# Kernel tuning notes

Hardware: AMD Instinct MI355X
Metric: run time of the kernel (lower is better)

Reference implementation:

```python
import jax, jax.numpy as jnp
import numpy as np

N_C = 64
D = 128

def setup_inputs() -> dict:
    key = jax.random.key(0)
    embeddings = jax.random.normal(key, (1024, N_C * D), dtype=jnp.float32)
    return {"embeddings": embeddings}

def reference(embeddings) -> jnp.ndarray:
    two_b, _ = embeddings.shape
    B = two_b // 2
    # (2, B, n_c, d), softmax over last dim
    q = jax.nn.softmax(embeddings.reshape(2, B, N_C, D), axis=-1)
    q_a, q_b = q[0], q[1]  # (B, n_c, d)

    self_sim_loss = -(q_a * q_b).sum() / (B * N_C)

    q_a2 = q_a * q_a
    q_b2 = q_b * q_b
    # Faithful to the repeat/repeat_interleave + bmm: block (i, j) of the
    # (n_c^2, d, d) product equals q2[:, j].T @ q2[:, i]  -> einsum over batch.
    prod_a = jnp.einsum('bjc,bid->ijcd', q_a2, q_a2)  # (n_c, n_c, d, d)
    prod_b = jnp.einsum('bjc,bid->ijcd', q_b2, q_b2)

    # mask out diagonal cluster pairs i == j (done before sqrt in original;
    # entries are strictly positive so masking after sqrt is identical)
    offdiag = (~jnp.eye(N_C, dtype=bool))[:, :, None, None]  # (n_c, n_c, 1, 1)

    raw_a = jnp.where(offdiag, jnp.sqrt(prod_a), 0.0).sum()
    raw_b = jnp.where(offdiag, jnp.sqrt(prod_b), 0.0).sum()

    scale = (N_C * N_C - N_C) * (B ** 0.5)
    cluster_loss = -(raw_a / scale + raw_b / scale) / 2
    return self_sim_loss + cluster_loss
```

## Files before the change

kernel.cpp:

```cpp
#include <hip/hip_runtime.h>
#include <cstdint>
#include <cstddef>

#define NCLUS 64
#define DIM   128
#define BATCH 512
#define QCOLS 8192
#define NPAIR 2016
#define TSTRB (QCOLS * BATCH)
#define FP8SCALE 256.0f

typedef float f32x16 __attribute__((ext_vector_type(16)));
typedef int   i32x4  __attribute__((ext_vector_type(4)));
typedef int   i32x8  __attribute__((ext_vector_type(8)));


__device__ __forceinline__ void ld_lds16(const void* g, void* l) {
  __builtin_amdgcn_global_load_lds(
      (__attribute__((address_space(1))) void*)g,
      (__attribute__((address_space(3))) void*)l, 16, 0, 0);
}

#define SYNC_VM4()  asm volatile("s_waitcnt vmcnt(4)\n\ts_barrier" ::: "memory")
#define SYNC_VM0()  asm volatile("s_waitcnt vmcnt(0)\n\ts_barrier" ::: "memory")
#define SYNC_LGKM() asm volatile("s_waitcnt lgkmcnt(0)\n\ts_barrier" ::: "memory")

__global__ __launch_bounds__(256) void softmax_q2_kernel(
    const float* __restrict__ emb, uint8_t* __restrict__ q2t,
    float* __restrict__ dotPart) {
  __shared__ uint32_t T32[2 * 64 * 33];
  __shared__ float red[4];
  const int c  = blockIdx.y;
  const int bq = blockIdx.x;
  const int tid = threadIdx.x;
  const int w = tid >> 6, lane = tid & 63;
  const int sub = lane >> 5;
  const int col = lane & 31;

  float4 qa = {0.f, 0.f, 0.f, 0.f};
  float dot = 0.f;

#pragma unroll
  for (int k = 0; k < 16; ++k) {
    const int t  = k & 1;
    const int bl = w * 16 + (k >> 1) * 2 + sub;
    const int b  = bq * 64 + bl;
    const float4 v = *(const float4*)(emb +
        ((size_t)(t * BATCH + b) * QCOLS + (size_t)c * DIM + col * 4));

    float mx = fmaxf(fmaxf(v.x, v.y), fmaxf(v.z, v.w));
#pragma unroll
    for (int off = 1; off < 32; off <<= 1) mx = fmaxf(mx, __shfl_xor(mx, off));
    float e0 = __expf(v.x - mx), e1 = __expf(v.y - mx);
    float e2 = __expf(v.z - mx), e3 = __expf(v.w - mx);
    float s = (e0 + e1) + (e2 + e3);
#pragma unroll
    for (int off = 1; off < 32; off <<= 1) s += __shfl_xor(s, off);
    const float inv = 1.0f / s;
    const float q0 = e0 * inv, q1 = e1 * inv, q2 = e2 * inv, q3 = e3 * inv;

    if (t == 0) { qa.x = q0; qa.y = q1; qa.z = q2; qa.w = q3; }
    else        { dot += qa.x * q0 + qa.y * q1 + qa.z * q2 + qa.w * q3; }

    int pk = __builtin_amdgcn_cvt_pk_fp8_f32(q0 * q0 * FP8SCALE,
                                             q1 * q1 * FP8SCALE, 0, false);
    pk = __builtin_amdgcn_cvt_pk_fp8_f32(q2 * q2 * FP8SCALE,
                                         q3 * q3 * FP8SCALE, pk, true);
    T32[(t * 64 + bl) * 33 + col] = (uint32_t)pk;
  }
  __syncthreads();

#pragma unroll
  for (int it = 0; it < 4; ++it) {
    int ch = it * 256 + tid;
    int t = ch >> 9, d = (ch >> 2) & 127, b16 = ch & 3;
    const int dq = d >> 2, sh = (d & 3) * 8;
    uint32_t w0 = 0, w1 = 0, w2 = 0, w3 = 0;
#pragma unroll
    for (int r = 0; r < 4; ++r) {
      w0 |= ((T32[(t * 64 + b16 * 16 +  0 + r) * 33 + dq] >> sh) & 0xFFu) << (8 * r);
      w1 |= ((T32[(t * 64 + b16 * 16 +  4 + r) * 33 + dq] >> sh) & 0xFFu) << (8 * r);
      w2 |= ((T32[(t * 64 + b16 * 16 +  8 + r) * 33 + dq] >> sh) & 0xFFu) << (8 * r);
      w3 |= ((T32[(t * 64 + b16 * 16 + 12 + r) * 33 + dq] >> sh) & 0xFFu) << (8 * r);
    }
    size_t off = (size_t)t * TSTRB + (size_t)(c * DIM + d) * BATCH +
                 (size_t)bq * 64 + b16 * 16;
    uint4 o; o.x = w0; o.y = w1; o.z = w2; o.w = w3;
    *(uint4*)(q2t + off) = o;
  }

#pragma unroll
  for (int off = 1; off < 64; off <<= 1) dot += __shfl_xor(dot, off);
  if (lane == 0) red[w] = dot;
  __syncthreads();
  if (tid == 0) dotPart[blockIdx.y * 8 + blockIdx.x] = red[0] + red[1] + red[2] + red[3];
}

__global__ __launch_bounds__(256, 4) void gram_sqrt_kernel(
    const uint8_t* __restrict__ q2t, float* __restrict__ Spart) {
  __shared__ uint8_t L[32768 + 16];

  int sidx = ((int)blockIdx.x & 7) * 252 + ((int)blockIdx.x >> 3);
  int q = sidx, gi = 0;
  while (q >= 64 * gi + 28) { q -= 64 * gi + 28; ++gi; }
  int I, J;
  if (q < 64 * gi) {
    int gj = q >> 6, r = q & 63;
    I = gi * 8 + (r >> 3);
    J = gj * 8 + (r & 7);
  } else {
    int dq = q - 64 * gi;
    int il = 1;
    while (il * (il + 1) / 2 <= dq) ++il;
    I = gi * 8 + il;
    J = gi * 8 + (dq - il * (il - 1) / 2);
  }

  const uint8_t* baseA = q2t + (size_t)J * (DIM * BATCH);
  const uint8_t* baseB = q2t + (size_t)I * (DIM * BATCH);

  const int tid  = threadIdx.x;
  const int lane = tid & 63, w = tid >> 6;
  const int wm = w & 1, wn = w >> 1;

  const int t0 = tid, t1 = 256 + tid;
  const int r0s = t0 >> 2, r1s = t1 >> 2;
  const int rot0 = (r0s + (r0s >> 2)) & 3;
  const int rot1 = (r1s + (r1s >> 2)) & 3;
  const int c0s = ((t0 & 3) - rot0) & 3;
  const int c1s = ((t1 & 3) - rot1) & 3;
  const size_t g0 = (size_t)r0s * BATCH + c0s * 16;
  const size_t g1 = (size_t)r1s * BATCH + c1s * 16;
  uint8_t* Lb = L;
  const int ldsw = w * 1024;

  const int h = lane >> 5, r31 = lane & 31;
  const int rot = (r31 + (r31 >> 2)) & 3;
  const int ro1 = ((2 * h + rot) & 3) * 16;
  const int ro2 = ((2 * h + 1 + rot) & 3) * 16;
  const int ArowO = (wm * 64 + r31) * 64;
  const int BrowO = 8192 + (wn * 64 + r31) * 64;

  f32x16 acc[2][2];
#pragma unroll
  for (int i = 0; i < 2; ++i)
#pragma unroll
    for (int j = 0; j < 2; ++j) acc[i][j] = (f32x16)(0.f);

  float S0 = 0.f, S1 = 0.f;

  ld_lds16(baseA + g0, Lb + ldsw);
  ld_lds16(baseA + g1, Lb + 4096 + ldsw);
  ld_lds16(baseB + g0, Lb + 8192 + ldsw);
  ld_lds16(baseB + g1, Lb + 12288 + ldsw);

  for (int m = 0; m < 16; ++m) {
    if (m < 15) {
      const int mi = m + 1;
      const int bb = (mi & 1) << 14;
      const size_t ck = (size_t)(mi >> 3) * TSTRB + (size_t)(mi & 7) * 64;
      ld_lds16(baseA + ck + g0, Lb + bb + ldsw);
      ld_lds16(baseA + ck + g1, Lb + bb + 4096 + ldsw);
      ld_lds16(baseB + ck + g0, Lb + bb + 8192 + ldsw);
      ld_lds16(baseB + ck + g1, Lb + bb + 12288 + ldsw);
      SYNC_VM4();
    } else {
      SYNC_VM0();
    }

    const int be = (m & 1) << 14;
    i32x4 alo[2], ahi[2], blo[2], bhi[2];
#pragma unroll
    for (int g = 0; g < 2; ++g) {
      alo[g] = *(const i32x4*)(Lb + be + ArowO + g * 2048 + ro1);
      ahi[g] = *(const i32x4*)(Lb + be + ArowO + g * 2048 + ro2);
      blo[g] = *(const i32x4*)(Lb + be + BrowO + g * 2048 + ro1);
      bhi[g] = *(const i32x4*)(Lb + be + BrowO + g * 2048 + ro2);
    }
    i32x8 af[2], bf[2];
#pragma unroll
    for (int g = 0; g < 2; ++g) {
      af[g] = (i32x8){alo[g].x, alo[g].y, alo[g].z, alo[g].w,
                      ahi[g].x, ahi[g].y, ahi[g].z, ahi[g].w};
      bf[g] = (i32x8){blo[g].x, blo[g].y, blo[g].z, blo[g].w,
                      bhi[g].x, bhi[g].y, bhi[g].z, bhi[g].w};
    }
#pragma unroll
    for (int i = 0; i < 2; ++i)
#pragma unroll
      for (int j = 0; j < 2; ++j)
        acc[i][j] = __builtin_amdgcn_mfma_scale_f32_32x32x64_f8f6f4(
            af[i], bf[j], acc[i][j], 0, 0, 0, 0x7F7F7F7F, 0, 0x7F7F7F7F);

    if (m == 7) {
#pragma unroll
      for (int i = 0; i < 2; ++i)
#pragma unroll
        for (int j = 0; j < 2; ++j) {
#pragma unroll
          for (int e = 0; e < 16; ++e) S0 += sqrtf(acc[i][j][e]);
          acc[i][j] = (f32x16)(0.f);
        }
    }

    SYNC_LGKM();
  }

#pragma unroll
  for (int i = 0; i < 2; ++i)
#pragma unroll
    for (int j = 0; j < 2; ++j)
#pragma unroll
      for (int e = 0; e < 16; ++e) S1 += sqrtf(acc[i][j][e]);

  float local = (S0 + S1) * (1.0f / 256.0f);
#pragma unroll
  for (int off = 1; off < 64; off <<= 1) local += __shfl_xor(local, off);
  float* fred = (float*)(L + 32768);
  if (lane == 0) fred[w] = local;
  __syncthreads();
  if (tid == 0) Spart[blockIdx.x] = fred[0] + fred[1] + fred[2] + fred[3];
}

__global__ __launch_bounds__(256) void finalize_kernel(
    const float* __restrict__ P, float* __restrict__ out) {
  __shared__ float rd[8];
  const int tid = threadIdx.x;
  float d = 0.f, s = 0.f;
  for (int i = tid; i < 512; i += 256) d += P[i];
  for (int i = tid; i < NPAIR; i += 256) s += P[512 + i];
#pragma unroll
  for (int off = 1; off < 64; off <<= 1) { d += __shfl_xor(d, off); s += __shfl_xor(s, off); }
  const int w = tid >> 6;
  if ((tid & 63) == 0) { rd[w] = d; rd[4 + w] = s; }
  __syncthreads();
  if (tid == 0) {
    float dt = rd[0] + rd[1] + rd[2] + rd[3];
    float st = rd[4] + rd[5] + rd[6] + rd[7];
    out[0] = -dt / 32768.0f - st / (4032.0f * 22.62741699796952f);
  }
}

extern "C" void kernel_launch(void* const* d_in, const int* in_sizes, int n_in,
                              void* d_out, int out_size, void* d_ws, size_t ws_size,
                              hipStream_t stream) {
  const float* emb = (const float*)d_in[0];
  float* out = (float*)d_out;
  float* P = (float*)d_ws;
  uint8_t* q2t = (uint8_t*)d_ws + 16384;

  softmax_q2_kernel<<<dim3(8, 64), 256, 0, stream>>>(emb, q2t, P);
  gram_sqrt_kernel<<<dim3(NPAIR), 256, 0, stream>>>(q2t, P + 512);
  finalize_kernel<<<1, 256, 0, stream>>>(P, out);
}
```

Before: 127.5 us.

## Load gram MFMA operands directly from global into registers, shrink softmax blocks

The gram kernel no longer stages fp8 tiles through LDS with async global-to-LDS loads and barriers. Each wave now loads its MFMA fragments straight from global memory into registers, double-buffered across 8 K-chunks of 128 bytes, which removes the LDS round trip and per-iteration barriers. The softmax kernel is split into 4x more blocks, each handling 16 batch rows, to raise parallelism, and the finalize offsets are adjusted to match. The costs are more register pressure from the 32 i32x4 fragment registers, less coalesced global reads, and loss of cross-wave operand sharing, so A and B tiles are fetched redundantly per wave.

```diff
diff --git a/kernel.cpp b/kernel.cpp
--- a/kernel.cpp
+++ b/kernel.cpp
@@ -15,20 +15,10 @@
 typedef int   i32x8  __attribute__((ext_vector_type(8)));
 
 
-__device__ __forceinline__ void ld_lds16(const void* g, void* l) {
-  __builtin_amdgcn_global_load_lds(
-      (__attribute__((address_space(1))) void*)g,
-      (__attribute__((address_space(3))) void*)l, 16, 0, 0);
-}
-
-#define SYNC_VM4()  asm volatile("s_waitcnt vmcnt(4)\n\ts_barrier" ::: "memory")
-#define SYNC_VM0()  asm volatile("s_waitcnt vmcnt(0)\n\ts_barrier" ::: "memory")
-#define SYNC_LGKM() asm volatile("s_waitcnt lgkmcnt(0)\n\ts_barrier" ::: "memory")
-
 __global__ __launch_bounds__(256) void softmax_q2_kernel(
     const float* __restrict__ emb, uint8_t* __restrict__ q2t,
     float* __restrict__ dotPart) {
-  __shared__ uint32_t T32[2 * 64 * 33];
+  __shared__ uint32_t T32[2 * 16 * 33];
   __shared__ float red[4];
   const int c  = blockIdx.y;
   const int bq = blockIdx.x;
@@ -41,10 +31,10 @@
   float dot = 0.f;
 
 #pragma unroll
-  for (int k = 0; k < 16; ++k) {
+  for (int k = 0; k < 4; ++k) {
     const int t  = k & 1;
-    const int bl = w * 16 + (k >> 1) * 2 + sub;
-    const int b  = bq * 64 + bl;
+    const int bl = w * 4 + (k >> 1) * 2 + sub;
+    const int b  = bq * 16 + bl;
     const float4 v = *(const float4*)(emb +
         ((size_t)(t * BATCH + b) * QCOLS + (size_t)c * DIM + col * 4));
 
@@ -66,25 +56,23 @@
                                              q1 * q1 * FP8SCALE, 0, false);
     pk = __builtin_amdgcn_cvt_pk_fp8_f32(q2 * q2 * FP8SCALE,
                                          q3 * q3 * FP8SCALE, pk, true);
-    T32[(t * 64 + bl) * 33 + col] = (uint32_t)pk;
-  }
-  __syncthreads();
-
-#pragma unroll
-  for (int it = 0; it < 4; ++it) {
-    int ch = it * 256 + tid;
-    int t = ch >> 9, d = (ch >> 2) & 127, b16 = ch & 3;
+    T32[(t * 16 + bl) * 33 + col] = (uint32_t)pk;
+  }
+  __syncthreads();
+
+  {
+    const int t = tid >> 7, d = tid & 127;
     const int dq = d >> 2, sh = (d & 3) * 8;
     uint32_t w0 = 0, w1 = 0, w2 = 0, w3 = 0;
 #pragma unroll
     for (int r = 0; r < 4; ++r) {
-      w0 |= ((T32[(t * 64 + b16 * 16 +  0 + r) * 33 + dq] >> sh) & 0xFFu) << (8 * r);
-      w1 |= ((T32[(t * 64 + b16 * 16 +  4 + r) * 33 + dq] >> sh) & 0xFFu) << (8 * r);
-      w2 |= ((T32[(t * 64 + b16 * 16 +  8 + r) * 33 + dq] >> sh) & 0xFFu) << (8 * r);
-      w3 |= ((T32[(t * 64 + b16 * 16 + 12 + r) * 33 + dq] >> sh) & 0xFFu) << (8 * r);
+      w0 |= ((T32[(t * 16 +  0 + r) * 33 + dq] >> sh) & 0xFFu) << (8 * r);
+      w1 |= ((T32[(t * 16 +  4 + r) * 33 + dq] >> sh) & 0xFFu) << (8 * r);
+      w2 |= ((T32[(t * 16 +  8 + r) * 33 + dq] >> sh) & 0xFFu) << (8 * r);
+      w3 |= ((T32[(t * 16 + 12 + r) * 33 + dq] >> sh) & 0xFFu) << (8 * r);
     }
     size_t off = (size_t)t * TSTRB + (size_t)(c * DIM + d) * BATCH +
-                 (size_t)bq * 64 + b16 * 16;
+                 (size_t)bq * 16;
     uint4 o; o.x = w0; o.y = w1; o.z = w2; o.w = w3;
     *(uint4*)(q2t + off) = o;
   }
@@ -93,12 +81,12 @@
   for (int off = 1; off < 64; off <<= 1) dot += __shfl_xor(dot, off);
   if (lane == 0) red[w] = dot;
   __syncthreads();
-  if (tid == 0) dotPart[blockIdx.y * 8 + blockIdx.x] = red[0] + red[1] + red[2] + red[3];
-}
-
-__global__ __launch_bounds__(256, 4) void gram_sqrt_kernel(
+  if (tid == 0) dotPart[c * 32 + bq] = red[0] + red[1] + red[2] + red[3];
+}
+
+__global__ __launch_bounds__(256) void gram_sqrt_kernel(
     const uint8_t* __restrict__ q2t, float* __restrict__ Spart) {
-  __shared__ uint8_t L[32768 + 16];
+  __shared__ float red[4];
 
   int sidx = ((int)blockIdx.x & 7) * 252 + ((int)blockIdx.x >> 3);
   int q = sidx, gi = 0;
@@ -116,30 +104,19 @@
     J = gi * 8 + (dq - il * (il - 1) / 2);
   }
 
-  const uint8_t* baseA = q2t + (size_t)J * (DIM * BATCH);
-  const uint8_t* baseB = q2t + (size_t)I * (DIM * BATCH);
+  const uint8_t* __restrict__ pA = q2t + (size_t)J * (DIM * BATCH);
+  const uint8_t* __restrict__ pB = q2t + (size_t)I * (DIM * BATCH);
 
   const int tid  = threadIdx.x;
   const int lane = tid & 63, w = tid >> 6;
   const int wm = w & 1, wn = w >> 1;
-
-  const int t0 = tid, t1 = 256 + tid;
-  const int r0s = t0 >> 2, r1s = t1 >> 2;
-  const int rot0 = (r0s + (r0s >> 2)) & 3;
-  const int rot1 = (r1s + (r1s >> 2)) & 3;
-  const int c0s = ((t0 & 3) - rot0) & 3;
-  const int c1s = ((t1 & 3) - rot1) & 3;
-  const size_t g0 = (size_t)r0s * BATCH + c0s * 16;
-  const size_t g1 = (size_t)r1s * BATCH + c1s * 16;
-  uint8_t* Lb = L;
-  const int ldsw = w * 1024;
-
   const int h = lane >> 5, r31 = lane & 31;
-  const int rot = (r31 + (r31 >> 2)) & 3;
-  const int ro1 = ((2 * h + rot) & 3) * 16;
-  const int ro2 = ((2 * h + 1 + rot) & 3) * 16;
-  const int ArowO = (wm * 64 + r31) * 64;
-  const int BrowO = 8192 + (wn * 64 + r31) * 64;
+  const uint32_t kb = (uint32_t)h * 32u;
+
+  const uint32_t oA0 = (uint32_t)(wm * 64 +  0 + r31) * BATCH + kb;
+  const uint32_t oA1 = (uint32_t)(wm * 64 + 32 + r31) * BATCH + kb;
+  const uint32_t oB0 = (uint32_t)(wn * 64 +  0 + r31) * BATCH + kb;
+  const uint32_t oB1 = (uint32_t)(wn * 64 + 32 + r31) * BATCH + kb;
 
   f32x16 acc[2][2];
 #pragma unroll
@@ -147,52 +124,57 @@
 #pragma unroll
     for (int j = 0; j < 2; ++j) acc[i][j] = (f32x16)(0.f);
 
+  i32x4 fr[2][16];
+
+#define CHOFF(p) ((size_t)((p) >> 2) * TSTRB + (size_t)((p) & 3) * 128)
+#define LD16(ptr) (*(const i32x4*)(ptr))
+#define ISSUE(sl, p) do {                                                   \
+    const uint8_t* ap = pA + CHOFF(p);                                      \
+    const uint8_t* bp = pB + CHOFF(p);                                      \
+    fr[sl][ 0] = LD16(ap + oA0);      fr[sl][ 1] = LD16(ap + oA0 + 16);     \
+    fr[sl][ 2] = LD16(ap + oA0 + 64); fr[sl][ 3] = LD16(ap + oA0 + 80);     \
+    fr[sl][ 4] = LD16(ap + oA1);      fr[sl][ 5] = LD16(ap + oA1 + 16);     \
+    fr[sl][ 6] = LD16(ap + oA1 + 64); fr[sl][ 7] = LD16(ap + oA1 + 80);     \
+    fr[sl][ 8] = LD16(bp + oB0);      fr[sl][ 9] = LD16(bp + oB0 + 16);     \
+    fr[sl][10] = LD16(bp + oB0 + 64); fr[sl][11] = LD16(bp + oB0 + 80);     \
+    fr[sl][12] = LD16(bp + oB1);      fr[sl][13] = LD16(bp + oB1 + 16);     \
+    fr[sl][14] = LD16(bp + oB1 + 64); fr[sl][15] = LD16(bp + oB1 + 80);     \
+  } while (0)
+
+#define MFMA(a, b, c) __builtin_amdgcn_mfma_scale_f32_32x32x64_f8f6f4(        \
+    (a), (b), (c), 0, 0, 0, 0x7F7F7F7F, 0, 0x7F7F7F7F)
+#define CAT8(lo, hi) __builtin_shufflevector((lo), (hi), 0, 1, 2, 3, 4, 5, 6, 7)
+
   float S0 = 0.f, S1 = 0.f;
 
-  ld_lds16(baseA + g0, Lb + ldsw);
-  ld_lds16(baseA + g1, Lb + 4096 + ldsw);
-  ld_lds16(baseB + g0, Lb + 8192 + ldsw);
-  ld_lds16(baseB + g1, Lb + 12288 + ldsw);
-
-  for (int m = 0; m < 16; ++m) {
-    if (m < 15) {
-      const int mi = m + 1;
-      const int bb = (mi & 1) << 14;
-      const size_t ck = (size_t)(mi >> 3) * TSTRB + (size_t)(mi & 7) * 64;
-      ld_lds16(baseA + ck + g0, Lb + bb + ldsw);
-      ld_lds16(baseA + ck + g1, Lb + bb + 4096 + ldsw);
-      ld_lds16(baseB + ck + g0, Lb + bb + 8192 + ldsw);
-      ld_lds16(baseB + ck + g1, Lb + bb + 12288 + ldsw);
-      SYNC_VM4();
-    } else {
-      SYNC_VM0();
-    }
-
-    const int be = (m & 1) << 14;
-    i32x4 alo[2], ahi[2], blo[2], bhi[2];
-#pragma unroll
-    for (int g = 0; g < 2; ++g) {
-      alo[g] = *(const i32x4*)(Lb + be + ArowO + g * 2048 + ro1);
-      ahi[g] = *(const i32x4*)(Lb + be + ArowO + g * 2048 + ro2);
-      blo[g] = *(const i32x4*)(Lb + be + BrowO + g * 2048 + ro1);
-      bhi[g] = *(const i32x4*)(Lb + be + BrowO + g * 2048 + ro2);
-    }
-    i32x8 af[2], bf[2];
-#pragma unroll
-    for (int g = 0; g < 2; ++g) {
-      af[g] = (i32x8){alo[g].x, alo[g].y, alo[g].z, alo[g].w,
-                      ahi[g].x, ahi[g].y, ahi[g].z, ahi[g].w};
-      bf[g] = (i32x8){blo[g].x, blo[g].y, blo[g].z, blo[g].w,
-                      bhi[g].x, bhi[g].y, bhi[g].z, bhi[g].w};
-    }
-#pragma unroll
-    for (int i = 0; i < 2; ++i)
-#pragma unroll
-      for (int j = 0; j < 2; ++j)
-        acc[i][j] = __builtin_amdgcn_mfma_scale_f32_32x32x64_f8f6f4(
-            af[i], bf[j], acc[i][j], 0, 0, 0, 0x7F7F7F7F, 0, 0x7F7F7F7F);
-
-    if (m == 7) {
+  ISSUE(0, 0);
+#pragma unroll
+  for (int p = 0; p < 8; ++p) {
+    if (p < 7) ISSUE((p + 1) & 1, p + 1);
+    const int sl = p & 1;
+
+    {
+      i32x8 a0 = CAT8(fr[sl][0],  fr[sl][1]);
+      i32x8 a1 = CAT8(fr[sl][4],  fr[sl][5]);
+      i32x8 b0 = CAT8(fr[sl][8],  fr[sl][9]);
+      i32x8 b1 = CAT8(fr[sl][12], fr[sl][13]);
+      acc[0][0] = MFMA(a0, b0, acc[0][0]);
+      acc[0][1] = MFMA(a0, b1, acc[0][1]);
+      acc[1][0] = MFMA(a1, b0, acc[1][0]);
+      acc[1][1] = MFMA(a1, b1, acc[1][1]);
+    }
+    {
+      i32x8 a0 = CAT8(fr[sl][2],  fr[sl][3]);
+      i32x8 a1 = CAT8(fr[sl][6],  fr[sl][7]);
+      i32x8 b0 = CAT8(fr[sl][10], fr[sl][11]);
+      i32x8 b1 = CAT8(fr[sl][14], fr[sl][15]);
+      acc[0][0] = MFMA(a0, b0, acc[0][0]);
+      acc[0][1] = MFMA(a0, b1, acc[0][1]);
+      acc[1][0] = MFMA(a1, b0, acc[1][0]);
+      acc[1][1] = MFMA(a1, b1, acc[1][1]);
+    }
+
+    if (p == 3) {
 #pragma unroll
       for (int i = 0; i < 2; ++i)
 #pragma unroll
@@ -202,8 +184,6 @@
           acc[i][j] = (f32x16)(0.f);
         }
     }
-
-    SYNC_LGKM();
   }
 
 #pragma unroll
@@ -216,10 +196,9 @@
   float local = (S0 + S1) * (1.0f / 256.0f);
 #pragma unroll
   for (int off = 1; off < 64; off <<= 1) local += __shfl_xor(local, off);
-  float* fred = (float*)(L + 32768);
-  if (lane == 0) fred[w] = local;
-  __syncthreads();
-  if (tid == 0) Spart[blockIdx.x] = fred[0] + fred[1] + fred[2] + fred[3];
+  if (lane == 0) red[w] = local;
+  __syncthreads();
+  if (tid == 0) Spart[blockIdx.x] = red[0] + red[1] + red[2] + red[3];
 }
 
 __global__ __launch_bounds__(256) void finalize_kernel(
@@ -227,8 +206,8 @@
   __shared__ float rd[8];
   const int tid = threadIdx.x;
   float d = 0.f, s = 0.f;
-  for (int i = tid; i < 512; i += 256) d += P[i];
-  for (int i = tid; i < NPAIR; i += 256) s += P[512 + i];
+  for (int i = tid; i < 2048; i += 256) d += P[i];
+  for (int i = tid; i < NPAIR; i += 256) s += P[2048 + i];
 #pragma unroll
   for (int off = 1; off < 64; off <<= 1) { d += __shfl_xor(d, off); s += __shfl_xor(s, off); }
   const int w = tid >> 6;
@@ -249,7 +228,7 @@
   float* P = (float*)d_ws;
   uint8_t* q2t = (uint8_t*)d_ws + 16384;
 
-  softmax_q2_kernel<<<dim3(8, 64), 256, 0, stream>>>(emb, q2t, P);
-  gram_sqrt_kernel<<<dim3(NPAIR), 256, 0, stream>>>(q2t, P + 512);
+  softmax_q2_kernel<<<dim3(32, 64), 256, 0, stream>>>(emb, q2t, P);
+  gram_sqrt_kernel<<<dim3(NPAIR), 256, 0, stream>>>(q2t, P + 2048);
   finalize_kernel<<<1, 256, 0, stream>>>(P, out);
 }
```

Result: slower. 202.6 us (+58.9%).

## Triple-buffer gram LDS pipeline, drop trailing barrier, widen softmax blocks

Applied to the files above, without the earlier changes.

The gram kernel moves from a double-buffered to a triple-buffered LDS pipeline with prefetch distance two. Each iteration now needs only one vmcnt wait plus barrier, because the end-of-iteration lgkmcnt barrier is gone, and the MFMA block runs at raised wave priority. The cost is 48KB of LDS per block and the loss of the 4-blocks-per-CU launch bound, which may lower occupancy. The softmax kernel also switches to 512-thread blocks, each doing half as many rows per thread.

```diff
diff --git a/kernel.cpp b/kernel.cpp
--- a/kernel.cpp
+++ b/kernel.cpp
@@ -21,15 +21,14 @@
       (__attribute__((address_space(3))) void*)l, 16, 0, 0);
 }
 
-#define SYNC_VM4()  asm volatile("s_waitcnt vmcnt(4)\n\ts_barrier" ::: "memory")
-#define SYNC_VM0()  asm volatile("s_waitcnt vmcnt(0)\n\ts_barrier" ::: "memory")
-#define SYNC_LGKM() asm volatile("s_waitcnt lgkmcnt(0)\n\ts_barrier" ::: "memory")
-
-__global__ __launch_bounds__(256) void softmax_q2_kernel(
+#define VM4_BAR() asm volatile("s_waitcnt vmcnt(4)\n\ts_barrier" ::: "memory")
+#define VM0_BAR() asm volatile("s_waitcnt vmcnt(0)\n\ts_barrier" ::: "memory")
+
+__global__ __launch_bounds__(512) void softmax_q2_kernel(
     const float* __restrict__ emb, uint8_t* __restrict__ q2t,
     float* __restrict__ dotPart) {
   __shared__ uint32_t T32[2 * 64 * 33];
-  __shared__ float red[4];
+  __shared__ float red[8];
   const int c  = blockIdx.y;
   const int bq = blockIdx.x;
   const int tid = threadIdx.x;
@@ -41,9 +40,9 @@
   float dot = 0.f;
 
 #pragma unroll
-  for (int k = 0; k < 16; ++k) {
+  for (int k = 0; k < 8; ++k) {
     const int t  = k & 1;
-    const int bl = w * 16 + (k >> 1) * 2 + sub;
+    const int bl = w * 8 + (k >> 1) * 2 + sub;
     const int b  = bq * 64 + bl;
     const float4 v = *(const float4*)(emb +
         ((size_t)(t * BATCH + b) * QCOLS + (size_t)c * DIM + col * 4));
@@ -71,8 +70,8 @@
   __syncthreads();
 
 #pragma unroll
-  for (int it = 0; it < 4; ++it) {
-    int ch = it * 256 + tid;
+  for (int it = 0; it < 2; ++it) {
+    int ch = it * 512 + tid;
     int t = ch >> 9, d = (ch >> 2) & 127, b16 = ch & 3;
     const int dq = d >> 2, sh = (d & 3) * 8;
     uint32_t w0 = 0, w1 = 0, w2 = 0, w3 = 0;
@@ -93,12 +92,17 @@
   for (int off = 1; off < 64; off <<= 1) dot += __shfl_xor(dot, off);
   if (lane == 0) red[w] = dot;
   __syncthreads();
-  if (tid == 0) dotPart[blockIdx.y * 8 + blockIdx.x] = red[0] + red[1] + red[2] + red[3];
-}
-
-__global__ __launch_bounds__(256, 4) void gram_sqrt_kernel(
+  if (tid == 0) {
+    float dt = 0.f;
+#pragma unroll
+    for (int i = 0; i < 8; ++i) dt += red[i];
+    dotPart[blockIdx.y * 8 + blockIdx.x] = dt;
+  }
+}
+
+__global__ __launch_bounds__(256) void gram_sqrt_kernel(
     const uint8_t* __restrict__ q2t, float* __restrict__ Spart) {
-  __shared__ uint8_t L[32768 + 16];
+  __shared__ uint8_t L[3 * 16384 + 16];
 
   int sidx = ((int)blockIdx.x & 7) * 252 + ((int)blockIdx.x >> 3);
   int q = sidx, gi = 0;
@@ -149,26 +153,26 @@
 
   float S0 = 0.f, S1 = 0.f;
 
-  ld_lds16(baseA + g0, Lb + ldsw);
-  ld_lds16(baseA + g1, Lb + 4096 + ldsw);
-  ld_lds16(baseB + g0, Lb + 8192 + ldsw);
-  ld_lds16(baseB + g1, Lb + 12288 + ldsw);
-
+#define CHOFF64(i) ((size_t)((i) >> 3) * TSTRB + (size_t)((i) & 7) * 64)
+#define STAGE(bufb, ck) do {                                       \
+    ld_lds16(baseA + (ck) + g0, Lb + (bufb) + ldsw);               \
+    ld_lds16(baseA + (ck) + g1, Lb + (bufb) + 4096 + ldsw);        \
+    ld_lds16(baseB + (ck) + g0, Lb + (bufb) + 8192 + ldsw);        \
+    ld_lds16(baseB + (ck) + g1, Lb + (bufb) + 12288 + ldsw);       \
+  } while (0)
+#define MFMA(a, b, c) __builtin_amdgcn_mfma_scale_f32_32x32x64_f8f6f4(        \
+    (a), (b), (c), 0, 0, 0, 0x7F7F7F7F, 0, 0x7F7F7F7F)
+
+  STAGE(0, CHOFF64(0));
+  STAGE(16384, CHOFF64(1));
+
+#pragma unroll
   for (int m = 0; m < 16; ++m) {
-    if (m < 15) {
-      const int mi = m + 1;
-      const int bb = (mi & 1) << 14;
-      const size_t ck = (size_t)(mi >> 3) * TSTRB + (size_t)(mi & 7) * 64;
-      ld_lds16(baseA + ck + g0, Lb + bb + ldsw);
-      ld_lds16(baseA + ck + g1, Lb + bb + 4096 + ldsw);
-      ld_lds16(baseB + ck + g0, Lb + bb + 8192 + ldsw);
-      ld_lds16(baseB + ck + g1, Lb + bb + 12288 + ldsw);
-      SYNC_VM4();
-    } else {
-      SYNC_VM0();
-    }
-
-    const int be = (m & 1) << 14;
+    if (m < 15) VM4_BAR(); else VM0_BAR();
+
+    if (m < 14) STAGE(((m + 2) % 3) * 16384, CHOFF64(m + 2));
+
+    const int be = (m % 3) * 16384;
     i32x4 alo[2], ahi[2], blo[2], bhi[2];
 #pragma unroll
     for (int g = 0; g < 2; ++g) {
@@ -185,12 +189,13 @@
       bf[g] = (i32x8){blo[g].x, blo[g].y, blo[g].z, blo[g].w,
                       bhi[g].x, bhi[g].y, bhi[g].z, bhi[g].w};
     }
+    __builtin_amdgcn_s_setprio(1);
 #pragma unroll
     for (int i = 0; i < 2; ++i)
 #pragma unroll
       for (int j = 0; j < 2; ++j)
-        acc[i][j] = __builtin_amdgcn_mfma_scale_f32_32x32x64_f8f6f4(
-            af[i], bf[j], acc[i][j], 0, 0, 0, 0x7F7F7F7F, 0, 0x7F7F7F7F);
+        acc[i][j] = MFMA(af[i], bf[j], acc[i][j]);
+    __builtin_amdgcn_s_setprio(0);
 
     if (m == 7) {
 #pragma unroll
@@ -202,8 +207,6 @@
           acc[i][j] = (f32x16)(0.f);
         }
     }
-
-    SYNC_LGKM();
   }
 
 #pragma unroll
@@ -216,7 +219,7 @@
   float local = (S0 + S1) * (1.0f / 256.0f);
 #pragma unroll
   for (int off = 1; off < 64; off <<= 1) local += __shfl_xor(local, off);
-  float* fred = (float*)(L + 32768);
+  float* fred = (float*)(L + 3 * 16384);
   if (lane == 0) fred[w] = local;
   __syncthreads();
   if (tid == 0) Spart[blockIdx.x] = fred[0] + fred[1] + fred[2] + fred[3];
@@ -249,7 +252,7 @@
   float* P = (float*)d_ws;
   uint8_t* q2t = (uint8_t*)d_ws + 16384;
 
-  softmax_q2_kernel<<<dim3(8, 64), 256, 0, stream>>>(emb, q2t, P);
+  softmax_q2_kernel<<<dim3(8, 64), 512, 0, stream>>>(emb, q2t, P);
   gram_sqrt_kernel<<<dim3(NPAIR), 256, 0, stream>>>(q2t, P + 512);
   finalize_kernel<<<1, 256, 0, stream>>>(P, out);
 }
```

After: 126.6 us. No clear change (-0.7%).
